# Kernel optimization log

Measured on AMD Instinct MI355X. Metric: run time of the kernel, lower is better.

The kernel has to match this reference:

```python
import jax, jax.numpy as jnp
import numpy as np

DIM = 1024
N_HEADS = 16
HEAD_DIM = DIM // N_HEADS
HIDDEN = 4096  # round_up(4*DIM, 256)
ROPE_THETA = 10000.0
EPS = 1e-6


def setup_inputs() -> dict:
    key = jax.random.key(0)
    ks = jax.random.split(key, 10)
    s = 0.02
    return {
        "x": jax.random.normal(ks[0], (1, 4096, DIM), dtype=jnp.float32),
        "wq": jax.random.normal(ks[1], (DIM, DIM), dtype=jnp.float32) * s,
        "wk": jax.random.normal(ks[2], (DIM, DIM), dtype=jnp.float32) * s,
        "wv": jax.random.normal(ks[3], (DIM, DIM), dtype=jnp.float32) * s,
        "wo": jax.random.normal(ks[4], (DIM, DIM), dtype=jnp.float32) * s,
        "w1": jax.random.normal(ks[5], (HIDDEN, DIM), dtype=jnp.float32) * s,
        "w2": jax.random.normal(ks[6], (DIM, HIDDEN), dtype=jnp.float32) * s,
        "w3": jax.random.normal(ks[7], (HIDDEN, DIM), dtype=jnp.float32) * s,
        "g_attn": jnp.ones((DIM,), dtype=jnp.float32),
        "g_ffn": jnp.ones((DIM,), dtype=jnp.float32),
    }


def _rmsnorm(x, g):
    return x * jax.lax.rsqrt(jnp.mean(x * x, axis=-1, keepdims=True) + EPS) * g


def _rope_tables(seqlen):
    inv = 1.0 / (ROPE_THETA ** (jnp.arange(0, HEAD_DIM, 2, dtype=jnp.float32) / HEAD_DIM))
    ang = jnp.arange(seqlen, dtype=jnp.float32)[:, None] * inv[None, :]  # [s, hd/2]
    return jnp.cos(ang), jnp.sin(ang)


def _apply_rope(q, cos, sin):
    # q: [b, s, h, hd]; pairs (even, odd) treated as complex (re, im)
    b, s, h, d = q.shape
    qr = q.reshape(b, s, h, d // 2, 2)
    re, im = qr[..., 0], qr[..., 1]
    c = cos[None, :, None, :]
    sn = sin[None, :, None, :]
    out = jnp.stack([re * c - im * sn, re * sn + im * c], axis=-1)
    return out.reshape(b, s, h, d)


def reference(x, wq, wk, wv, wo, w1, w2, w3, g_attn, g_ffn):
    b, s, _ = x.shape
    xn = _rmsnorm(x, g_attn)
    q = (xn @ wq.T).reshape(b, s, N_HEADS, HEAD_DIM)
    k = (xn @ wk.T).reshape(b, s, N_HEADS, HEAD_DIM)
    v = (xn @ wv.T).reshape(b, s, N_HEADS, HEAD_DIM)
    cos, sin = _rope_tables(s)
    q = _apply_rope(q, cos, sin)
    k = _apply_rope(k, cos, sin)
    scores = jnp.einsum("bthd,bThd->bhtT", q, k) / np.sqrt(HEAD_DIM).astype(np.float32)
    probs = jax.nn.softmax(scores, axis=-1)
    attn = jnp.einsum("bhtT,bThd->bthd", probs, v).reshape(b, s, DIM)
    h = x + attn @ wo.T
    hn = _rmsnorm(h, g_ffn)
    ff = (jax.nn.silu(hn @ w1.T) * (hn @ w3.T)) @ w2.T
    return h + ff
```

## Files before the change

### kernel.cpp

```cpp
#include <hip/hip_runtime.h>

#define S_LEN 4096
#define DIMM  1024
#define NH    16
#define HD    64
#define HID   4096

typedef unsigned short u16;
typedef __attribute__((ext_vector_type(8))) short bf16x8;
typedef __attribute__((ext_vector_type(4))) short short4b;
typedef __attribute__((ext_vector_type(8))) unsigned short u16x8;
typedef __attribute__((ext_vector_type(4))) float f32x4;

__device__ __forceinline__ u16 f2bf(float f) {
  unsigned u = __float_as_uint(f);
  u += 0x7fffu + ((u >> 16) & 1u);
  return (u16)(u >> 16);
}
__device__ __forceinline__ float bf2f(u16 h) {
  return __uint_as_float(((unsigned)h) << 16);
}
__device__ __forceinline__ unsigned pack_bf16(float hi, float lo) {
  return __builtin_amdgcn_perm(__float_as_uint(hi), __float_as_uint(lo), 0x07060302u);
}
__device__ __forceinline__ float fexp2(float x) { return __builtin_amdgcn_exp2f(x); }

__device__ __forceinline__ void gl_lds16(const void* g, void* l) {
  __builtin_amdgcn_global_load_lds(
      (const __attribute__((address_space(1))) void*)g,
      (__attribute__((address_space(3))) void*)l, 16, 0, 0);
}

__device__ __forceinline__ f32x4 mfma16(short4b a, short4b b, f32x4 c) {
#if __has_builtin(__builtin_amdgcn_mfma_f32_16x16x16bf16_1k)
  return __builtin_amdgcn_mfma_f32_16x16x16bf16_1k(a, b, c, 0, 0, 0);
#else
  asm("v_mfma_f32_16x16x16_bf16 %0, %1, %2, %0" : "+v"(c) : "v"(a), "v"(b));
  return c;
#endif
}

__global__ __launch_bounds__(256) void prep_kernel(
    const float* __restrict__ wq, const float* __restrict__ wk, const float* __restrict__ wv,
    const float* __restrict__ wo, const float* __restrict__ w1, const float* __restrict__ w3,
    const float* __restrict__ w2, const float* __restrict__ x, const float* __restrict__ g_attn,
    u16* __restrict__ wqkb, u16* __restrict__ wvb, u16* __restrict__ wob,
    u16* __restrict__ w13b, u16* __restrict__ w2b, u16* __restrict__ xnb,
    float* __restrict__ cosT, float* __restrict__ sinT) {
  int b = blockIdx.x;
  int t = threadIdx.x;
  if (b < 8192) {
    const float* src;
    u16* dst;
    int i;
    if (b < 2048) {
      int which = b >> 9, lb = b & 511;
      src = which == 0 ? wq : which == 1 ? wk : which == 2 ? wv : wo;
      dst = which == 0 ? wqkb : which == 1 ? (wqkb + (1 << 20)) : which == 2 ? wvb : wob;
      i = (lb * 256 + t) * 8;
    } else {
      int b2 = b - 2048, which = b2 >> 11, lb = b2 & 2047;
      src = which == 0 ? w1 : which == 1 ? w3 : w2;
      dst = which == 0 ? w13b : which == 1 ? (w13b + (4 << 20)) : w2b;
      i = (lb * 256 + t) * 8;
    }
    float4 a = *(const float4*)(src + i);
    float4 c = *(const float4*)(src + i + 4);
    u16x8 r;
    r[0] = f2bf(a.x); r[1] = f2bf(a.y); r[2] = f2bf(a.z); r[3] = f2bf(a.w);
    r[4] = f2bf(c.x); r[5] = f2bf(c.y); r[6] = f2bf(c.z); r[7] = f2bf(c.w);
    *(u16x8*)(dst + i) = r;
  } else if (b < 8704) {
    int idx = (b - 8192) * 256 + t;
    int pos = idx >> 5, i = idx & 31;
    double inv = pow(10000.0, -(double)(2 * i) / 64.0);
    double a = (double)pos * inv;
    cosT[idx] = (float)cos(a);
    sinT[idx] = (float)sin(a);
  } else {
    int row = b - 8704;
    const float4 v = *(const float4*)(x + (size_t)row * DIMM + t * 4);
    float ss = v.x * v.x + v.y * v.y + v.z * v.z + v.w * v.w;
#pragma unroll
    for (int off = 32; off > 0; off >>= 1) ss += __shfl_down(ss, off);
    __shared__ float red[4];
    if ((t & 63) == 0) red[t >> 6] = ss;
    __syncthreads();
    float tot = red[0] + red[1] + red[2] + red[3];
    float sc = rsqrtf(tot * (1.0f / DIMM) + 1e-6f);
    const float4 gv = *(const float4*)(g_attn + t * 4);
    ushort4 o;
    o.x = f2bf(v.x * sc * gv.x);
    o.y = f2bf(v.y * sc * gv.y);
    o.z = f2bf(v.z * sc * gv.z);
    o.w = f2bf(v.w * sc * gv.w);
    *(ushort4*)(xnb + (size_t)row * DIMM + t * 4) = o;
  }
}

__global__ __launch_bounds__(256) void rmsnorm_kernel(const float* __restrict__ x, const float* __restrict__ g,
                                                      u16* __restrict__ out) {
  int row = blockIdx.x;
  int t = threadIdx.x;
  const float4 v = *(const float4*)(x + (size_t)row * DIMM + t * 4);
  float ss = v.x * v.x + v.y * v.y + v.z * v.z + v.w * v.w;
#pragma unroll
  for (int off = 32; off > 0; off >>= 1) ss += __shfl_down(ss, off);
  __shared__ float red[4];
  if ((t & 63) == 0) red[t >> 6] = ss;
  __syncthreads();
  float tot = red[0] + red[1] + red[2] + red[3];
  float sc = rsqrtf(tot * (1.0f / DIMM) + 1e-6f);
  const float4 gv = *(const float4*)(g + t * 4);
  ushort4 o;
  o.x = f2bf(v.x * sc * gv.x);
  o.y = f2bf(v.y * sc * gv.y);
  o.z = f2bf(v.z * sc * gv.z);
  o.w = f2bf(v.w * sc * gv.w);
  *(ushort4*)(out + (size_t)row * DIMM + t * 4) = o;
}

template <int OUTMODE>
__global__ __launch_bounds__(512) void gemm_kernel(const u16* __restrict__ A, const u16* __restrict__ B,
                                                   void* Cout, const float* res, int N, int K, int lda,
                                                   const float* cosT, const float* sinT) {
  __shared__ uint4 As[512];
  __shared__ uint4 Bs[512];
  const int t = threadIdx.x;
  const int w = t >> 6, l = t & 63;
  const int wm = w >> 1, wn = w & 1;
  const int bm = blockIdx.y, bn = blockIdx.x;
  const int quad = l >> 4, lc = l & 15;

  f32x4 acc[2][4];
  const f32x4 zero = {0.0f, 0.0f, 0.0f, 0.0f};
#pragma unroll
  for (int mi = 0; mi < 2; mi++)
#pragma unroll
    for (int ni = 0; ni < 4; ni++) acc[mi][ni] = zero;

  const int band0 = t >> 6, kq0 = (t >> 4) & 3, row0 = t & 15;
  const u16* Ap0 = A + (size_t)(bm * 128 + band0 * 16 + row0) * lda + kq0 * 8;
  const u16* Bp0 = B + (size_t)(bn * 128 + band0 * 16 + row0) * K + kq0 * 8;
  const int abase = wm * 128 + l;
  const int bbase = wn * 256 + l;

  for (int k0 = 0; k0 < K; k0 += 32) {
    gl_lds16(Ap0 + k0, &As[t]);
    gl_lds16(Bp0 + k0, &Bs[t]);
    __syncthreads();
    bf16x8 af[2], bfr[4];
#pragma unroll
    for (int mi = 0; mi < 2; mi++) af[mi] = *(const bf16x8*)&As[abase + mi * 64];
#pragma unroll
    for (int ni = 0; ni < 4; ni++) bfr[ni] = *(const bf16x8*)&Bs[bbase + ni * 64];
#pragma unroll
    for (int mi = 0; mi < 2; mi++)
#pragma unroll
      for (int ni = 0; ni < 4; ni++)
        acc[mi][ni] = __builtin_amdgcn_mfma_f32_16x16x32_bf16(af[mi], bfr[ni], acc[mi][ni], 0, 0, 0);
    __syncthreads();
  }

  const int rbase = bm * 128 + wm * 32 + quad * 4;
  const int cbase = bn * 128 + wn * 64 + lc;
#pragma unroll
  for (int mi = 0; mi < 2; mi++) {
#pragma unroll
    for (int r = 0; r < 4; r++) {
      int row = rbase + mi * 16 + r;
#pragma unroll
      for (int ni = 0; ni < 4; ni++) {
        int col = cbase + ni * 16;
        if constexpr (OUTMODE == 0) {
          ((u16*)Cout)[(size_t)row * N + col] = f2bf(acc[mi][ni][r]);
        } else if constexpr (OUTMODE == 1) {
          size_t idx = (size_t)row * N + col;
          ((float*)Cout)[idx] = res[idx] + acc[mi][ni][r];
        } else if constexpr (OUTMODE == 2) {
          int h = row >> 6, din = row & 63;
          int kb = col >> 6, k63 = col & 63;
          int off = ((h << 6) + kb) * 4096 + (((din >> 4) << 1) + (k63 >> 5)) * 512 +
                    ((((k63 >> 2) & 3) << 4) + (din & 15)) * 8 + ((k63 >> 4) & 1) * 4 + (k63 & 3);
          ((u16*)Cout)[off] = f2bf(acc[mi][ni][r]);
        } else {
          float v = acc[mi][ni][r];
          float pv = __shfl_xor(v, 1);
          int i = ((ni * 16 + lc) & 63) >> 1;
          float c = cosT[(row << 5) + i], s = sinT[(row << 5) + i];
          float o = (lc & 1) ? (pv * s + v * c) : (v * c - pv * s);
          ((u16*)Cout)[(size_t)row * N + col] = f2bf(o);
        }
      }
    }
  }
}

__global__ __launch_bounds__(512) void gemm256_kernel(const u16* __restrict__ A, const u16* __restrict__ B,
                                                      u16* __restrict__ Cout, int N, int K, int lda) {
  __shared__ uint4 As0[1024], Bs0[1024], As1[1024], Bs1[1024];
  const int t = threadIdx.x;
  const int w = t >> 6, l = t & 63;
  const int wm = w >> 2, wn = w & 3;
  const int bm = blockIdx.y, bn = blockIdx.x;
  const int quad = l >> 4, lc = l & 15;

  f32x4 acc[8][4];
  const f32x4 zero = {0.0f, 0.0f, 0.0f, 0.0f};
#pragma unroll
  for (int mi = 0; mi < 8; mi++)
#pragma unroll
    for (int ni = 0; ni < 4; ni++) acc[mi][ni] = zero;

  const int band0 = t >> 6, kq0 = (t >> 4) & 3, row0 = t & 15;
  const u16* Ap0 = A + (size_t)(bm * 256 + band0 * 16 + row0) * lda + kq0 * 8;
  const u16* Bp0 = B + (size_t)(bn * 256 + band0 * 16 + row0) * K + kq0 * 8;
  const size_t Astep = (size_t)128 * lda;
  const size_t Bstep = (size_t)128 * K;

#define STAGE256(AD, BD, K0)                      \
  do {                                            \
    gl_lds16(Ap0 + (K0), &(AD)[t]);               \
    gl_lds16(Ap0 + Astep + (K0), &(AD)[t + 512]); \
    gl_lds16(Bp0 + (K0), &(BD)[t]);               \
    gl_lds16(Bp0 + Bstep + (K0), &(BD)[t + 512]); \
  } while (0)

#define COMPUTE256(AS, BS)                                                                          \
  do {                                                                                              \
    bf16x8 af[8], bfr[4];                                                                           \
    _Pragma("unroll") for (int mi = 0; mi < 8; mi++)                                                \
        af[mi] = *(const bf16x8*)&(AS)[(wm * 8 + mi) * 64 + l];                                     \
    _Pragma("unroll") for (int ni = 0; ni < 4; ni++)                                                \
        bfr[ni] = *(const bf16x8*)&(BS)[(wn * 4 + ni) * 64 + l];                                    \
    _Pragma("unroll") for (int mi = 0; mi < 8; mi++)                                                \
        _Pragma("unroll") for (int ni = 0; ni < 4; ni++)                                            \
            acc[mi][ni] = __builtin_amdgcn_mfma_f32_16x16x32_bf16(af[mi], bfr[ni], acc[mi][ni], 0, 0, 0); \
  } while (0)

  STAGE256(As0, Bs0, 0);
  __syncthreads();

  int k0 = 0;
  for (; k0 + 64 < K; k0 += 64) {
    STAGE256(As1, Bs1, k0 + 32);
    COMPUTE256(As0, Bs0);
    __syncthreads();
    STAGE256(As0, Bs0, k0 + 64);
    COMPUTE256(As1, Bs1);
    __syncthreads();
  }
  STAGE256(As1, Bs1, k0 + 32);
  COMPUTE256(As0, Bs0);
  __syncthreads();
  COMPUTE256(As1, Bs1);
#undef STAGE256
#undef COMPUTE256

  const int rbase = bm * 256 + wm * 128 + quad * 4;
  const int cbase = bn * 256 + wn * 64 + lc;
#pragma unroll
  for (int mi = 0; mi < 8; mi++) {
#pragma unroll
    for (int r = 0; r < 4; r++) {
      int row = rbase + mi * 16 + r;
#pragma unroll
      for (int ni = 0; ni < 4; ni++) {
        int col = cbase + ni * 16;
        Cout[(size_t)row * N + col] = f2bf(acc[mi][ni][r]);
      }
    }
  }
}

__global__ __launch_bounds__(512) void attn_kernel(const u16* __restrict__ Qm, const u16* __restrict__ Km,
                                                   const u16* __restrict__ Vsw, u16* __restrict__ Om) {
  __shared__ char smem[32768];
  uint4* Ks0 = (uint4*)smem;
  uint4* Vs0 = (uint4*)(smem + 8192);
  uint4* Ks1 = (uint4*)(smem + 16384);
  uint4* Vs1 = (uint4*)(smem + 24576);
  const int t = threadIdx.x;
  const int w = t >> 6, l = t & 63;
  const int quad = l >> 4, lc = l & 15;
  const int hd = blockIdx.y;
  const int qrow = blockIdx.x * 128 + w * 16;

  bf16x8 qf_[2];
#pragma unroll
  for (int ch = 0; ch < 2; ch++)
    qf_[ch] = *(const bf16x8*)(Qm + (size_t)(qrow + lc) * 2048 + hd * HD + ch * 32 + quad * 8);

  const f32x4 zero = {0.0f, 0.0f, 0.0f, 0.0f};
  f32x4 Oa[4];
#pragma unroll
  for (int df = 0; df < 4; df++) Oa[df] = zero;
  float mt = -1e30f, ls = 0.0f;

  const int s0 = t >> 7, c0 = (t >> 6) & 1, kq0 = (t >> 4) & 3, row0 = t & 15;
  const u16* Kp0 = Km + (size_t)(s0 * 16 + row0) * 2048 + hd * HD + c0 * 32 + kq0 * 8;
  const u16* Vp = Vsw + (size_t)(hd * HD) * 4096 + t * 8;
  const float csc = 0.125f * 1.44269504088896f;

#define STAGEKV(KD, VD, TT)                                  \
  do {                                                       \
    gl_lds16(Kp0 + (size_t)(TT)*131072, &(KD)[t]);           \
    gl_lds16(Vp + (size_t)(TT)*4096, &(VD)[t]);              \
  } while (0)

#define TILE_COMPUTE(KS, VS)                                                                 \
  do {                                                                                       \
    f32x4 Sf[4];                                                                             \
    _Pragma("unroll") for (int kf = 0; kf < 4; kf++) {                                       \
      bf16x8 ka = *(const bf16x8*)&(KS)[kf * 128 + l];                                       \
      bf16x8 kb2 = *(const bf16x8*)&(KS)[kf * 128 + 64 + l];                                 \
      f32x4 z = __builtin_amdgcn_mfma_f32_16x16x32_bf16(ka, qf_[0], zero, 0, 0, 0);          \
      z = __builtin_amdgcn_mfma_f32_16x16x32_bf16(kb2, qf_[1], z, 0, 0, 0);                  \
      Sf[kf] = z * csc;                                                                      \
    }                                                                                        \
    float tmax = -1e30f;                                                                     \
    _Pragma("unroll") for (int kf = 0; kf < 4; kf++)                                         \
        _Pragma("unroll") for (int r = 0; r < 4; r++) tmax = fmaxf(tmax, Sf[kf][r]);         \
    tmax = fmaxf(tmax, __shfl_xor(tmax, 16));                                                \
    tmax = fmaxf(tmax, __shfl_xor(tmax, 32));                                                \
    if (!__all(tmax <= mt + 8.0f)) {                                                        \
      float mnew = fmaxf(mt, tmax);                                                          \
      float alpha = fexp2(mt - mnew);                                                        \
      mt = mnew;                                                                             \
      ls *= alpha;                                                                           \
      _Pragma("unroll") for (int df = 0; df < 4; df++) Oa[df] *= alpha;                      \
    }                                                                                        \
    float psum = 0.0f;                                                                       \
    _Pragma("unroll") for (int kf = 0; kf < 4; kf++)                                         \
        _Pragma("unroll") for (int r = 0; r < 4; r++) {                                      \
      float p = fexp2(Sf[kf][r] - mt);                                                       \
      Sf[kf][r] = p;                                                                         \
      psum += p;                                                                             \
    }                                                                                        \
    psum += __shfl_xor(psum, 16);                                                            \
    psum += __shfl_xor(psum, 32);                                                            \
    ls += psum;                                                                              \
    short4b pk[4];                                                                           \
    _Pragma("unroll") for (int kf = 0; kf < 4; kf++) {                                       \
      union { short4b s4; uint2 u2; } cv;                                                    \
      cv.u2.x = pack_bf16(Sf[kf][1], Sf[kf][0]);                                             \
      cv.u2.y = pack_bf16(Sf[kf][3], Sf[kf][2]);                                             \
      pk[kf] = cv.s4;                                                                        \
    }                                                                                        \
    _Pragma("unroll") for (int df = 0; df < 4; df++)                                         \
        _Pragma("unroll") for (int tp = 0; tp < 2; tp++) {                                   \
      union { bf16x8 v8; short4b h[2]; } vv;                                                 \
      vv.v8 = *(const bf16x8*)&(VS)[(df * 2 + tp) * 64 + l];                                 \
      Oa[df] = mfma16(vv.h[0], pk[2 * tp], Oa[df]);                                          \
      Oa[df] = mfma16(vv.h[1], pk[2 * tp + 1], Oa[df]);                                      \
    }                                                                                        \
  } while (0)

  STAGEKV(Ks0, Vs0, 0);
  __syncthreads();

  for (int tt = 0; tt < 64; tt += 2) {
    STAGEKV(Ks1, Vs1, tt + 1);
    TILE_COMPUTE(Ks0, Vs0);
    __syncthreads();
    if (tt + 2 < 64) STAGEKV(Ks0, Vs0, tt + 2);
    TILE_COMPUTE(Ks1, Vs1);
    __syncthreads();
  }
#undef STAGEKV
#undef TILE_COMPUTE

  u16* ep = (u16*)smem;
  float invl = 1.0f / ls;
#pragma unroll
  for (int df = 0; df < 4; df++) {
    int qb = w * 16 + lc;
    int d = df * 16 + quad * 4;
    uint2 pv;
    pv.x = pack_bf16(Oa[df][1] * invl, Oa[df][0] * invl);
    pv.y = pack_bf16(Oa[df][3] * invl, Oa[df][2] * invl);
    *(uint2*)(ep + qb * 72 + d) = pv;
  }
  __syncthreads();
#pragma unroll
  for (int it = 0; it < 2; it++) {
    int qb = it * 64 + (t >> 3);
    int dp = (t & 7) * 8;
    u16x8 rowv = *(const u16x8*)(ep + qb * 72 + dp);
    *(u16x8*)(Om + (size_t)(blockIdx.x * 128 + qb) * DIMM + hd * HD + dp) = rowv;
  }
}

__global__ __launch_bounds__(256) void silu_mul_kernel(u16* __restrict__ u13) {
  int i = (blockIdx.x * 256 + threadIdx.x) * 8;
  int r = i >> 12, c = i & 4095;
  u16* up = u13 + (size_t)r * 8192 + c;
  u16x8 uv = *(const u16x8*)up;
  u16x8 gv = *(const u16x8*)(up + 4096);
  u16x8 o;
#pragma unroll
  for (int j = 0; j < 8; j++) {
    float a = bf2f(uv[j]);
    float b = bf2f(gv[j]);
    float sv = a / (1.0f + __expf(-a));
    o[j] = f2bf(sv * b);
  }
  *(u16x8*)up = o;
}

extern "C" void kernel_launch(void* const* d_in, const int* in_sizes, int n_in,
                              void* d_out, int out_size, void* d_ws, size_t ws_size,
                              hipStream_t stream) {
  const float* x      = (const float*)d_in[0];
  const float* wq     = (const float*)d_in[1];
  const float* wk     = (const float*)d_in[2];
  const float* wv     = (const float*)d_in[3];
  const float* wo     = (const float*)d_in[4];
  const float* w1     = (const float*)d_in[5];
  const float* w2     = (const float*)d_in[6];
  const float* w3     = (const float*)d_in[7];
  const float* g_attn = (const float*)d_in[8];
  const float* g_ffn  = (const float*)d_in[9];
  float* out = (float*)d_out;
  char* ws = (char*)d_ws;
  const size_t MB = 1ull << 20;

  u16* wqkb = (u16*)(ws + 0 * MB);
  u16* wvb  = (u16*)(ws + 4 * MB);
  u16* wob  = (u16*)(ws + 6 * MB);
  u16* w13b = (u16*)(ws + 8 * MB);
  u16* w2b  = (u16*)(ws + 24 * MB);
  u16* xnb  = (u16*)(ws + 32 * MB);
  u16* qkb  = (u16*)(ws + 40 * MB);
  u16* vswz = (u16*)(ws + 56 * MB);
  u16* attb = (u16*)(ws + 64 * MB);
  u16* u13  = (u16*)(ws + 40 * MB);
  float* cosT = (float*)(ws + 104 * MB);
  float* sinT = (float*)(ws + 104 * MB + 512 * 1024);

  prep_kernel<<<12800, 256, 0, stream>>>(wq, wk, wv, wo, w1, w3, w2, x, g_attn,
                                         wqkb, wvb, wob, w13b, w2b, xnb, cosT, sinT);

  gemm_kernel<3><<<dim3(16, 32), 512, 0, stream>>>(xnb, wqkb, qkb, nullptr, 2048, DIMM, DIMM, cosT, sinT);
  gemm_kernel<2><<<dim3(32, 8), 512, 0, stream>>>(wvb, xnb, vswz, nullptr, S_LEN, DIMM, DIMM, nullptr, nullptr);

  attn_kernel<<<dim3(32, 16), 512, 0, stream>>>(qkb, qkb + 1024, vswz, attb);

  gemm_kernel<1><<<dim3(8, 32), 512, 0, stream>>>(attb, wob, out, x, DIMM, DIMM, DIMM, nullptr, nullptr);

  rmsnorm_kernel<<<4096, 256, 0, stream>>>(out, g_ffn, xnb);

  gemm256_kernel<<<dim3(32, 16), 512, 0, stream>>>(xnb, w13b, u13, 8192, DIMM, DIMM);

  silu_mul_kernel<<<8192, 256, 0, stream>>>(u13);

  gemm_kernel<1><<<dim3(8, 32), 512, 0, stream>>>(u13, w2b, out, out, DIMM, HID, 8192, nullptr, nullptr);
}
```

Before: 562.5 us.

## Double-buffer GEMM LDS tiles and widen K step to 64

The GEMM main loop moves from a single LDS buffer with two barriers per 32-wide K step to ping-pong buffers, each holding a 64-wide K slice. The global-to-LDS loads for the next slice are issued before the MFMAs on the current slice, so load latency can overlap compute, and barriers are halved. This quadruples LDS use to 64KB per block, which may reduce occupancy. The loop structure assumes K is a multiple of 128 and at least 128.

```diff
diff --git a/kernel.cpp b/kernel.cpp
--- a/kernel.cpp
+++ b/kernel.cpp
@@ -124,8 +124,7 @@
 __global__ __launch_bounds__(512) void gemm_kernel(const u16* __restrict__ A, const u16* __restrict__ B,
                                                    void* Cout, const float* res, int N, int K, int lda,
                                                    const float* cosT, const float* sinT) {
-  __shared__ uint4 As[512];
-  __shared__ uint4 Bs[512];
+  __shared__ uint4 As0[1024], Bs0[1024], As1[1024], Bs1[1024];
   const int t = threadIdx.x;
   const int w = t >> 6, l = t & 63;
   const int wm = w >> 1, wn = w & 1;
@@ -145,22 +144,45 @@
   const int abase = wm * 128 + l;
   const int bbase = wn * 256 + l;
 
-  for (int k0 = 0; k0 < K; k0 += 32) {
-    gl_lds16(Ap0 + k0, &As[t]);
-    gl_lds16(Bp0 + k0, &Bs[t]);
-    __syncthreads();
-    bf16x8 af[2], bfr[4];
-#pragma unroll
-    for (int mi = 0; mi < 2; mi++) af[mi] = *(const bf16x8*)&As[abase + mi * 64];
-#pragma unroll
-    for (int ni = 0; ni < 4; ni++) bfr[ni] = *(const bf16x8*)&Bs[bbase + ni * 64];
-#pragma unroll
-    for (int mi = 0; mi < 2; mi++)
-#pragma unroll
-      for (int ni = 0; ni < 4; ni++)
-        acc[mi][ni] = __builtin_amdgcn_mfma_f32_16x16x32_bf16(af[mi], bfr[ni], acc[mi][ni], 0, 0, 0);
-    __syncthreads();
-  }
+#define STAGEL(AD, BD, K0)                 \
+  do {                                     \
+    gl_lds16(Ap0 + (K0), &(AD)[t]);        \
+    gl_lds16(Ap0 + (K0) + 32, &(AD)[t + 512]); \
+    gl_lds16(Bp0 + (K0), &(BD)[t]);        \
+    gl_lds16(Bp0 + (K0) + 32, &(BD)[t + 512]); \
+  } while (0)
+
+#define COMPL(AS, BS)                                                                               \
+  do {                                                                                              \
+    _Pragma("unroll") for (int ks = 0; ks < 2; ks++) {                                              \
+      bf16x8 af[2], bfr[4];                                                                         \
+      _Pragma("unroll") for (int mi = 0; mi < 2; mi++)                                              \
+          af[mi] = *(const bf16x8*)&(AS)[ks * 512 + abase + mi * 64];                               \
+      _Pragma("unroll") for (int ni = 0; ni < 4; ni++)                                              \
+          bfr[ni] = *(const bf16x8*)&(BS)[ks * 512 + bbase + ni * 64];                              \
+      _Pragma("unroll") for (int mi = 0; mi < 2; mi++)                                              \
+          _Pragma("unroll") for (int ni = 0; ni < 4; ni++)                                          \
+              acc[mi][ni] = __builtin_amdgcn_mfma_f32_16x16x32_bf16(af[mi], bfr[ni], acc[mi][ni], 0, 0, 0); \
+    }                                                                                               \
+  } while (0)
+
+  STAGEL(As0, Bs0, 0);
+  __syncthreads();
+  int k0 = 0;
+  for (; k0 + 128 < K; k0 += 128) {
+    STAGEL(As1, Bs1, k0 + 64);
+    COMPL(As0, Bs0);
+    __syncthreads();
+    STAGEL(As0, Bs0, k0 + 128);
+    COMPL(As1, Bs1);
+    __syncthreads();
+  }
+  STAGEL(As1, Bs1, k0 + 64);
+  COMPL(As0, Bs0);
+  __syncthreads();
+  COMPL(As1, Bs1);
+#undef STAGEL
+#undef COMPL
 
   const int rbase = bm * 128 + wm * 32 + quad * 4;
   const int cbase = bn * 128 + wn * 64 + lc;
```

Result: faster. 536.0 us (-4.7%).
